# Kernel tuning notes

Measured on AMD Instinct MI355X. Metric: run time of the kernel, lower is better.

The kernel has to match this reference:

```python
import jax, jax.numpy as jnp
import numpy as np

N = 50000
E = 800000
HID = 128
EIN = 2 * HID + 1  # h[row] ++ h[col] ++ edge_attr
NC = 3             # n_coords
DIM = 3            # spatial dim
NORM_FACTOR = 100.0
LN_EPS = 1e-5


def layernorm(x, g, b):
    m = jnp.mean(x, axis=-1, keepdims=True)
    v = jnp.mean(jnp.square(x - m), axis=-1, keepdims=True)
    return (x - m) * jax.lax.rsqrt(v + LN_EPS) * g + b


def setup_inputs() -> dict:
    key = jax.random.key(0)
    ks = jax.random.split(key, 12)
    h = jax.random.normal(ks[0], (N, HID), dtype=jnp.float32)
    coord = jax.random.normal(ks[1], (N, NC, DIM), dtype=jnp.float32)
    coord_diff = jax.random.normal(ks[2], (E, NC, DIM), dtype=jnp.float32)
    edge_attr = jax.random.normal(ks[3], (E, 1), dtype=jnp.float32)
    edge_mask = jnp.ones((E, 1), dtype=jnp.float32)
    node_mask = jnp.ones((N, 1, 1), dtype=jnp.float32)
    row = jax.random.randint(ks[4], (E,), 0, N, dtype=jnp.int32)
    col = jax.random.randint(ks[5], (E,), 0, N, dtype=jnp.int32)
    # MLP params (stored [in, out])
    def xavier(k, fi, fo, gain=1.0):
        lim = gain * np.sqrt(6.0 / (fi + fo))
        return jax.random.uniform(k, (fi, fo), dtype=jnp.float32, minval=-lim, maxval=lim)
    W1 = xavier(ks[6], EIN, HID)
    b1 = jnp.zeros((HID,), jnp.float32)
    g1 = jnp.ones((HID,), jnp.float32)
    be1 = jnp.zeros((HID,), jnp.float32)
    W2 = xavier(ks[7], HID, HID)
    b2 = jnp.zeros((HID,), jnp.float32)
    g2 = jnp.ones((HID,), jnp.float32)
    be2 = jnp.zeros((HID,), jnp.float32)
    W3 = xavier(ks[8], HID, NC * NC, gain=0.01)  # final layer, no bias
    return dict(h=h, coord=coord, coord_diff=coord_diff, edge_attr=edge_attr,
                edge_mask=edge_mask, node_mask=node_mask, row=row, col=col,
                W1=W1, b1=b1, g1=g1, be1=be1, W2=W2, b2=b2, g2=g2, be2=be2, W3=W3)


def reference(h, coord, coord_diff, edge_attr, edge_mask, node_mask, row, col,
              W1, b1, g1, be1, W2, b2, g2, be2, W3):
    # gather node feats into edge features: [E, 2*HID + 1]
    x = jnp.concatenate([h[row], h[col], edge_attr], axis=1)
    x = jax.nn.silu(layernorm(x @ W1 + b1, g1, be1))
    x = jax.nn.silu(layernorm(x @ W2 + b2, g2, be2))
    phi = (x @ W3).reshape(-1, NC, NC)               # [E, NC, NC]
    trans = jnp.einsum('ejk,ejl->elk', coord_diff, phi)  # [E, NC, DIM]
    trans = trans * edge_mask[:, None]               # [E,1,1] broadcast
    agg = jax.ops.segment_sum(trans, row, num_segments=coord.shape[0]) / NORM_FACTOR
    return (coord + agg) * node_mask
```

## Files before the change

kernel.cpp:

```cpp
#include <hip/hip_runtime.h>
#include <hip/hip_bf16.h>

#define NN 50000
#define EE 800000

typedef __attribute__((ext_vector_type(8))) short short8;
typedef __attribute__((ext_vector_type(4))) float f32x4;

__device__ __forceinline__ float bf2f(ushort u) {
  union { unsigned u; float f; } v; v.u = ((unsigned)u) << 16; return v.f;
}
__device__ __forceinline__ ushort f2bf(float f) {
  union { float f; unsigned u; } v; v.f = f;
  unsigned r = v.u + 0x7FFFu + ((v.u >> 16) & 1u);
  return (ushort)(r >> 16);
}

__global__ void prep_kernel(const float* __restrict__ h, ushort* __restrict__ hb,
                            const float* __restrict__ W1, const float* __restrict__ W2,
                            const float* __restrict__ W3,
                            ushort* __restrict__ W1t, ushort* __restrict__ W2t,
                            ushort* __restrict__ W3t, float* __restrict__ agg) {
  int b = blockIdx.x, tid = threadIdx.x;
  if (b < 3125) {
    int i = b * 256 + tid;
    const float4* p = (const float4*)h;
    float4 a = p[2*i], c = p[2*i+1];
    short8 o;
    o[0]=f2bf(a.x); o[1]=f2bf(a.y); o[2]=f2bf(a.z); o[3]=f2bf(a.w);
    o[4]=f2bf(c.x); o[5]=f2bf(c.y); o[6]=f2bf(c.z); o[7]=f2bf(c.w);
    *(short8*)(hb + 8*i) = o;
  } else if (b < 3325) {
    int i = (b - 3125) * 256 + tid;
    if (i < 32768) {
      int n = i >> 8, k = i & 255;
      W1t[i] = f2bf(W1[k*128 + n]);
    } else if (i < 49152) {
      int j = i - 32768, n = j >> 7, k = j & 127;
      W2t[j] = f2bf(W2[k*128 + n]);
    } else if (i < 51200) {
      int j = i - 49152, n = j >> 7, k = j & 127;
      W3t[j] = (n < 9) ? f2bf(W3[k*9 + n]) : (ushort)0;
    }
  } else {
    int i = (b - 3325) * 256 + tid;
    if (i < NN*9) agg[i] = 0.f;
  }
}

__device__ __forceinline__ void ln_silu_inplace(ushort* smX, float* smRedS, float* smRedQ,
                                                const float* __restrict__ g,
                                                const float* __restrict__ be, int tid) {
  int e = tid & 63, w4 = tid >> 6, n0 = w4 * 32;
  float v[32]; float s = 0.f, q = 0.f;
  int bo[4];
  #pragma unroll
  for (int c = 0; c < 4; ++c) {
    bo[c] = (e*256 + (n0 + c*8)*2) ^ ((e & 7) << 4);
    short8 x = *(const short8*)((char*)smX + bo[c]);
    #pragma unroll
    for (int j = 0; j < 8; ++j) {
      float f = bf2f((ushort)x[j]); v[c*8+j] = f; s += f; q += f*f;
    }
  }
  smRedS[w4*64 + e] = s; smRedQ[w4*64 + e] = q;
  __syncthreads();
  s = smRedS[e] + smRedS[64+e] + smRedS[128+e] + smRedS[192+e];
  q = smRedQ[e] + smRedQ[64+e] + smRedQ[128+e] + smRedQ[192+e];
  float m  = s * (1.f/128.f);
  float rs = rsqrtf(q * (1.f/128.f) - m*m + 1e-5f);
  #pragma unroll
  for (int c = 0; c < 4; ++c) {
    short8 o;
    #pragma unroll
    for (int j = 0; j < 8; ++j) {
      float val = (v[c*8+j] - m) * rs * g[n0 + c*8 + j] + be[n0 + c*8 + j];
      val = val * __builtin_amdgcn_rcpf(1.f + __expf(-val));
      o[j] = f2bf(val);
    }
    *(short8*)((char*)smX + bo[c]) = o;
  }
  __syncthreads();
}

template<bool USE_HB>
__global__ __launch_bounds__(256, 4)
void edge_kernel(const float* __restrict__ h, const ushort* __restrict__ hb,
                 const ushort* __restrict__ W1t, const ushort* __restrict__ W2t,
                 const ushort* __restrict__ W3t,
                 const float* __restrict__ W1,
                 const float* __restrict__ b1, const float* __restrict__ g1, const float* __restrict__ be1,
                 const float* __restrict__ b2, const float* __restrict__ g2, const float* __restrict__ be2,
                 const float* __restrict__ edge_attr, const float* __restrict__ edge_mask,
                 const float* __restrict__ coord_diff,
                 const int* __restrict__ row, const int* __restrict__ col,
                 float* __restrict__ agg) {
  __shared__ __align__(16) char smem[35840];
  ushort* smA   = (ushort*)smem;
  ushort* smX   = (ushort*)smem;
  float*  smRedS = (float*)(smem + 16384);
  float*  smRedQ = (float*)(smem + 17408);
  float*  smPhi  = (float*)(smem + 18432);
  float*  smCd   = (float*)(smem + 32768);
  float*  smEA   = (float*)(smem + 35072);
  float*  smEM   = (float*)(smem + 35328);
  int*    smRow  = (int*)  (smem + 35584);

  const int tid  = threadIdx.x;
  const int lane = tid & 63;
  const int w    = tid >> 6;
  const int l15  = lane & 15;
  const int lh   = lane >> 4;
  const int wm   = w >> 1;
  const int wn   = w & 1;
  const int e0   = blockIdx.x * 64;

  {
    int e = tid >> 2, p = tid & 3;
    int re = row[e0 + e], ce = col[e0 + e];
    if (p == 0) { smEA[e] = edge_attr[e0+e]; smEM[e] = edge_mask[e0+e]; smRow[e] = re; }
    if (USE_HB) {
      const ushort* s = hb + (size_t)((p & 2) ? ce : re) * 128 + (p & 1) * 64;
      #pragma unroll
      for (int c = 0; c < 8; ++c) {
        short8 v = *(const short8*)(s + c*8);
        int bo = (e*512 + (p*8 + c)*16) ^ ((e & 7) << 4);
        *(short8*)((char*)smA + bo) = v;
      }
    } else {
      const float* s = h + (size_t)((p & 2) ? ce : re) * 128 + (p & 1) * 64;
      #pragma unroll
      for (int c = 0; c < 8; ++c) {
        float4 a = *(const float4*)(s + c*8);
        float4 bq = *(const float4*)(s + c*8 + 4);
        short8 v;
        v[0]=f2bf(a.x); v[1]=f2bf(a.y); v[2]=f2bf(a.z); v[3]=f2bf(a.w);
        v[4]=f2bf(bq.x); v[5]=f2bf(bq.y); v[6]=f2bf(bq.z); v[7]=f2bf(bq.w);
        int bo = (e*512 + (p*8 + c)*16) ^ ((e & 7) << 4);
        *(short8*)((char*)smA + bo) = v;
      }
    }
  }
  if (tid < 144)
    *(float4*)(smCd + tid*4) = *(const float4*)(coord_diff + (size_t)e0*9 + tid*4);
  __syncthreads();

  f32x4 acc[2][4] = {};
  {
    const ushort* Wp[4];
    #pragma unroll
    for (int nf = 0; nf < 4; ++nf)
      Wp[nf] = W1t + (size_t)(wn*64 + nf*16 + l15) * 256 + lh*8;
    #pragma unroll
    for (int k0 = 0; k0 < 8; ++k0) {
      short8 b[4];
      #pragma unroll
      for (int nf = 0; nf < 4; ++nf) b[nf] = *(const short8*)(Wp[nf] + k0*32);
      #pragma unroll
      for (int mi = 0; mi < 2; ++mi) {
        int r = wm*32 + mi*16 + l15;
        int bo = (r*512 + k0*64 + lh*16) ^ ((r & 7) << 4);
        short8 a = *(const short8*)((char*)smA + bo);
        #pragma unroll
        for (int nf = 0; nf < 4; ++nf)
          acc[mi][nf] = __builtin_amdgcn_mfma_f32_16x16x32_bf16(a, b[nf], acc[mi][nf], 0, 0, 0);
      }
    }
  }
  __syncthreads();

  {
    const float* w1last = W1 + 256*128;
    float bbv[4], wlv[4];
    #pragma unroll
    for (int nf = 0; nf < 4; ++nf) {
      int n = wn*64 + nf*16 + l15;
      bbv[nf] = b1[n]; wlv[nf] = w1last[n];
    }
    #pragma unroll
    for (int mi = 0; mi < 2; ++mi) {
      int r0 = wm*32 + mi*16 + lh*4;
      float ea[4];
      #pragma unroll
      for (int j = 0; j < 4; ++j) ea[j] = smEA[r0 + j];
      #pragma unroll
      for (int nf = 0; nf < 4; ++nf) {
        int n = wn*64 + nf*16 + l15;
        #pragma unroll
        for (int j = 0; j < 4; ++j) {
          int r = r0 + j;
          float val = acc[mi][nf][j] + bbv[nf] + ea[j] * wlv[nf];
          *(ushort*)((char*)smX + ((r*256 + n*2) ^ ((r & 7) << 4))) = f2bf(val);
        }
      }
    }
  }
  __syncthreads();
  ln_silu_inplace(smX, smRedS, smRedQ, g1, be1, tid);

  f32x4 acc2[2][4] = {};
  {
    const ushort* Wp[4];
    #pragma unroll
    for (int nf = 0; nf < 4; ++nf)
      Wp[nf] = W2t + (size_t)(wn*64 + nf*16 + l15) * 128 + lh*8;
    #pragma unroll
    for (int k0 = 0; k0 < 4; ++k0) {
      short8 b[4];
      #pragma unroll
      for (int nf = 0; nf < 4; ++nf) b[nf] = *(const short8*)(Wp[nf] + k0*32);
      #pragma unroll
      for (int mi = 0; mi < 2; ++mi) {
        int r = wm*32 + mi*16 + l15;
        int bo = (r*256 + k0*64 + lh*16) ^ ((r & 7) << 4);
        short8 a = *(const short8*)((char*)smX + bo);
        #pragma unroll
        for (int nf = 0; nf < 4; ++nf)
          acc2[mi][nf] = __builtin_amdgcn_mfma_f32_16x16x32_bf16(a, b[nf], acc2[mi][nf], 0, 0, 0);
      }
    }
  }
  __syncthreads();

  {
    float bbv[4];
    #pragma unroll
    for (int nf = 0; nf < 4; ++nf) bbv[nf] = b2[wn*64 + nf*16 + l15];
    #pragma unroll
    for (int mi = 0; mi < 2; ++mi) {
      int r0 = wm*32 + mi*16 + lh*4;
      #pragma unroll
      for (int nf = 0; nf < 4; ++nf) {
        int n = wn*64 + nf*16 + l15;
        #pragma unroll
        for (int j = 0; j < 4; ++j) {
          int r = r0 + j;
          float val = acc2[mi][nf][j] + bbv[nf];
          *(ushort*)((char*)smX + ((r*256 + n*2) ^ ((r & 7) << 4))) = f2bf(val);
        }
      }
    }
  }
  __syncthreads();
  ln_silu_inplace(smX, smRedS, smRedQ, g2, be2, tid);

  {
    f32x4 acc3 = {};
    const ushort* Wp = W3t + (size_t)l15*128 + lh*8;
    #pragma unroll
    for (int k0 = 0; k0 < 4; ++k0) {
      short8 b = *(const short8*)(Wp + k0*32);
      int r = w*16 + l15;
      int bo = (r*256 + k0*64 + lh*16) ^ ((r & 7) << 4);
      short8 a = *(const short8*)((char*)smX + bo);
      acc3 = __builtin_amdgcn_mfma_f32_16x16x32_bf16(a, b, acc3, 0, 0, 0);
    }
    if (l15 < 9) {
      #pragma unroll
      for (int j = 0; j < 4; ++j)
        smPhi[(w*16 + lh*4 + j)*12 + l15] = acc3[j];
    }
  }
  __syncthreads();

  {
    int e = tid >> 2, qd = tid & 3;
    int re = smRow[e];
    float em = smEM[e];
    const float* cd = smCd + e*9;
    const float* ph = smPhi + e*12;
    for (int idx = qd; idx < 9; idx += 4) {
      int l2 = idx / 3, k = idx - l2*3;
      float t = cd[k]*ph[l2] + cd[3+k]*ph[3+l2] + cd[6+k]*ph[6+l2];
      unsafeAtomicAdd(&agg[(size_t)re*9 + idx], t * em);
    }
  }
}

__global__ void finalize_kernel(const float* __restrict__ coord, const float* __restrict__ node_mask,
                                const float* __restrict__ agg, float* __restrict__ out) {
  int i = blockIdx.x * 256 + threadIdx.x;
  if (i < NN*9) {
    int n = i / 9;
    out[i] = (coord[i] + agg[i] * 0.01f) * node_mask[n];
  }
}

extern "C" void kernel_launch(void* const* d_in, const int* in_sizes, int n_in,
                              void* d_out, int out_size, void* d_ws, size_t ws_size,
                              hipStream_t stream) {
  const float* h          = (const float*)d_in[0];
  const float* coord      = (const float*)d_in[1];
  const float* coord_diff = (const float*)d_in[2];
  const float* edge_attr  = (const float*)d_in[3];
  const float* edge_mask  = (const float*)d_in[4];
  const float* node_mask  = (const float*)d_in[5];
  const int*   rowi       = (const int*)d_in[6];
  const int*   coli       = (const int*)d_in[7];
  const float* W1  = (const float*)d_in[8];
  const float* b1  = (const float*)d_in[9];
  const float* g1  = (const float*)d_in[10];
  const float* be1 = (const float*)d_in[11];
  const float* W2  = (const float*)d_in[12];
  const float* b2  = (const float*)d_in[13];
  const float* g2  = (const float*)d_in[14];
  const float* be2 = (const float*)d_in[15];
  const float* W3  = (const float*)d_in[16];

  char* ws = (char*)d_ws;
  float*  agg = (float*)ws;
  ushort* W1t = (ushort*)(ws + 1800064);
  ushort* W2t = (ushort*)(ws + 1865600);
  ushort* W3t = (ushort*)(ws + 1898368);
  ushort* hb  = (ushort*)(ws + 1902464);
  bool use_hb = ws_size >= (size_t)1902464 + 12800000;

  if (use_hb) {
    prep_kernel<<<3325 + (NN*9 + 255)/256, 256, 0, stream>>>(h, hb, W1, W2, W3, W1t, W2t, W3t, agg);
    edge_kernel<true><<<EE/64, 256, 0, stream>>>(h, hb, W1t, W2t, W3t, W1,
        b1, g1, be1, b2, g2, be2, edge_attr, edge_mask, coord_diff, rowi, coli, agg);
  } else {
    prep_kernel<<<3325 + (NN*9 + 255)/256, 256, 0, stream>>>(h, hb, W1, W2, W3, W1t, W2t, W3t, agg);
    edge_kernel<false><<<EE/64, 256, 0, stream>>>(h, hb, W1t, W2t, W3t, W1,
        b1, g1, be1, b2, g2, be2, edge_attr, edge_mask, coord_diff, rowi, coli, agg);
  }
  finalize_kernel<<<(NN*9 + 255)/256, 256, 0, stream>>>(coord, node_mask, agg, (float*)d_out);
}
```

Baseline: 519.7 us.

## Transpose MFMA roles and fuse bias/LayerNorm/SiLU into register epilogues

The MLP GEMMs are re-oriented so weights become the A operand (read from global) and edge activations the B operand from LDS. Each lane then holds four consecutive hidden features per edge. That lets the bias, edge-attr term, LayerNorm statistics and SiLU run directly on accumulator registers, with shuffle reductions and a small cross-wave LDS exchange. This removes the separate bf16 round-trip through LDS before each LayerNorm and several block barriers. The cost is more global weight loads per wave and a different LDS access pattern for the activations.

```diff
diff --git a/kernel.cpp b/kernel.cpp
--- a/kernel.cpp
+++ b/kernel.cpp
@@ -5,6 +5,7 @@
 #define EE 800000
 
 typedef __attribute__((ext_vector_type(8))) short short8;
+typedef __attribute__((ext_vector_type(4))) short short4v;
 typedef __attribute__((ext_vector_type(4))) float f32x4;
 
 __device__ __forceinline__ float bf2f(ushort u) {
@@ -14,6 +15,9 @@
   union { float f; unsigned u; } v; v.f = f;
   unsigned r = v.u + 0x7FFFu + ((v.u >> 16) & 1u);
   return (ushort)(r >> 16);
+}
+__device__ __forceinline__ float silu(float v) {
+  return v * __builtin_amdgcn_rcpf(1.f + __expf(-v));
 }
 
 __global__ void prep_kernel(const float* __restrict__ h, ushort* __restrict__ hb,
@@ -48,41 +52,6 @@
   }
 }
 
-__device__ __forceinline__ void ln_silu_inplace(ushort* smX, float* smRedS, float* smRedQ,
-                                                const float* __restrict__ g,
-                                                const float* __restrict__ be, int tid) {
-  int e = tid & 63, w4 = tid >> 6, n0 = w4 * 32;
-  float v[32]; float s = 0.f, q = 0.f;
-  int bo[4];
-  #pragma unroll
-  for (int c = 0; c < 4; ++c) {
-    bo[c] = (e*256 + (n0 + c*8)*2) ^ ((e & 7) << 4);
-    short8 x = *(const short8*)((char*)smX + bo[c]);
-    #pragma unroll
-    for (int j = 0; j < 8; ++j) {
-      float f = bf2f((ushort)x[j]); v[c*8+j] = f; s += f; q += f*f;
-    }
-  }
-  smRedS[w4*64 + e] = s; smRedQ[w4*64 + e] = q;
-  __syncthreads();
-  s = smRedS[e] + smRedS[64+e] + smRedS[128+e] + smRedS[192+e];
-  q = smRedQ[e] + smRedQ[64+e] + smRedQ[128+e] + smRedQ[192+e];
-  float m  = s * (1.f/128.f);
-  float rs = rsqrtf(q * (1.f/128.f) - m*m + 1e-5f);
-  #pragma unroll
-  for (int c = 0; c < 4; ++c) {
-    short8 o;
-    #pragma unroll
-    for (int j = 0; j < 8; ++j) {
-      float val = (v[c*8+j] - m) * rs * g[n0 + c*8 + j] + be[n0 + c*8 + j];
-      val = val * __builtin_amdgcn_rcpf(1.f + __expf(-val));
-      o[j] = f2bf(val);
-    }
-    *(short8*)((char*)smX + bo[c]) = o;
-  }
-  __syncthreads();
-}
-
 template<bool USE_HB>
 __global__ __launch_bounds__(256, 4)
 void edge_kernel(const float* __restrict__ h, const ushort* __restrict__ hb,
@@ -95,16 +64,15 @@
                  const float* __restrict__ coord_diff,
                  const int* __restrict__ row, const int* __restrict__ col,
                  float* __restrict__ agg) {
-  __shared__ __align__(16) char smem[35840];
+  __shared__ __align__(16) char smem[36864];
   ushort* smA   = (ushort*)smem;
   ushort* smX   = (ushort*)smem;
-  float*  smRedS = (float*)(smem + 16384);
-  float*  smRedQ = (float*)(smem + 17408);
-  float*  smPhi  = (float*)(smem + 18432);
-  float*  smCd   = (float*)(smem + 32768);
-  float*  smEA   = (float*)(smem + 35072);
-  float*  smEM   = (float*)(smem + 35328);
-  int*    smRow  = (int*)  (smem + 35584);
+  float*  smPhi = (float*)(smem + 16384);
+  float*  smCd  = (float*)(smem + 32768);
+  float*  smEA  = (float*)(smem + 35072);
+  float*  smEM  = (float*)(smem + 35328);
+  int*    smRow = (int*)  (smem + 35584);
+  float2* smRed = (float2*)(smem + 35840);
 
   const int tid  = threadIdx.x;
   const int lane = tid & 63;
@@ -115,6 +83,8 @@
   const int wn   = w & 1;
   const int e0   = blockIdx.x * 64;
 
+  const int nb = wm*64 + lh*4;
+
   {
     int e = tid >> 2, p = tid & 3;
     int re = row[e0 + e], ce = col[e0 + e];
@@ -145,121 +115,175 @@
     *(float4*)(smCd + tid*4) = *(const float4*)(coord_diff + (size_t)e0*9 + tid*4);
   __syncthreads();
 
-  f32x4 acc[2][4] = {};
-  {
-    const ushort* Wp[4];
-    #pragma unroll
-    for (int nf = 0; nf < 4; ++nf)
-      Wp[nf] = W1t + (size_t)(wn*64 + nf*16 + l15) * 256 + lh*8;
+  f32x4 acc[4][2] = {};
+  {
+    const ushort* A0 = W1t + (size_t)(wm*64 + l15) * 256 + lh*8;
     #pragma unroll
     for (int k0 = 0; k0 < 8; ++k0) {
-      short8 b[4];
-      #pragma unroll
-      for (int nf = 0; nf < 4; ++nf) b[nf] = *(const short8*)(Wp[nf] + k0*32);
-      #pragma unroll
-      for (int mi = 0; mi < 2; ++mi) {
-        int r = wm*32 + mi*16 + l15;
-        int bo = (r*512 + k0*64 + lh*16) ^ ((r & 7) << 4);
-        short8 a = *(const short8*)((char*)smA + bo);
-        #pragma unroll
-        for (int nf = 0; nf < 4; ++nf)
-          acc[mi][nf] = __builtin_amdgcn_mfma_f32_16x16x32_bf16(a, b[nf], acc[mi][nf], 0, 0, 0);
-      }
-    }
-  }
-  __syncthreads();
-
-  {
-    const float* w1last = W1 + 256*128;
-    float bbv[4], wlv[4];
-    #pragma unroll
-    for (int nf = 0; nf < 4; ++nf) {
-      int n = wn*64 + nf*16 + l15;
-      bbv[nf] = b1[n]; wlv[nf] = w1last[n];
-    }
-    #pragma unroll
-    for (int mi = 0; mi < 2; ++mi) {
-      int r0 = wm*32 + mi*16 + lh*4;
-      float ea[4];
-      #pragma unroll
-      for (int j = 0; j < 4; ++j) ea[j] = smEA[r0 + j];
-      #pragma unroll
-      for (int nf = 0; nf < 4; ++nf) {
-        int n = wn*64 + nf*16 + l15;
+      short8 a[4], b[2];
+      #pragma unroll
+      for (int mf = 0; mf < 4; ++mf) a[mf] = *(const short8*)(A0 + mf*4096 + k0*32);
+      #pragma unroll
+      for (int nf = 0; nf < 2; ++nf) {
+        int e = wn*32 + nf*16 + l15;
+        int bo = (e*512 + k0*64 + lh*16) ^ ((e & 7) << 4);
+        b[nf] = *(const short8*)((char*)smA + bo);
+      }
+      #pragma unroll
+      for (int mf = 0; mf < 4; ++mf)
+        #pragma unroll
+        for (int nf = 0; nf < 2; ++nf)
+          acc[mf][nf] = __builtin_amdgcn_mfma_f32_16x16x32_bf16(a[mf], b[nf], acc[mf][nf], 0, 0, 0);
+    }
+  }
+
+  float s[2] = {0.f, 0.f}, q[2] = {0.f, 0.f};
+  {
+    const float* wl = W1 + 256*128;
+    float ea[2];
+    #pragma unroll
+    for (int nf = 0; nf < 2; ++nf) ea[nf] = smEA[wn*32 + nf*16 + l15];
+    #pragma unroll
+    for (int mf = 0; mf < 4; ++mf) {
+      float4 b1q = *(const float4*)(b1 + nb + mf*16);
+      float4 wlq = *(const float4*)(wl + nb + mf*16);
+      #pragma unroll
+      for (int nf = 0; nf < 2; ++nf)
         #pragma unroll
         for (int j = 0; j < 4; ++j) {
-          int r = r0 + j;
-          float val = acc[mi][nf][j] + bbv[nf] + ea[j] * wlv[nf];
-          *(ushort*)((char*)smX + ((r*256 + n*2) ^ ((r & 7) << 4))) = f2bf(val);
+          float t = acc[mf][nf][j] + ((const float*)&b1q)[j] + ea[nf] * ((const float*)&wlq)[j];
+          acc[mf][nf][j] = t; s[nf] += t; q[nf] += t*t;
         }
-      }
-    }
-  }
-  __syncthreads();
-  ln_silu_inplace(smX, smRedS, smRedQ, g1, be1, tid);
-
-  f32x4 acc2[2][4] = {};
-  {
-    const ushort* Wp[4];
-    #pragma unroll
-    for (int nf = 0; nf < 4; ++nf)
-      Wp[nf] = W2t + (size_t)(wn*64 + nf*16 + l15) * 128 + lh*8;
+    }
+  }
+  #pragma unroll
+  for (int nf = 0; nf < 2; ++nf) {
+    s[nf] += __shfl_xor(s[nf], 16, 64); s[nf] += __shfl_xor(s[nf], 32, 64);
+    q[nf] += __shfl_xor(q[nf], 16, 64); q[nf] += __shfl_xor(q[nf], 32, 64);
+  }
+  if (lh == 0) {
+    #pragma unroll
+    for (int nf = 0; nf < 2; ++nf)
+      smRed[((wm*2 + wn)*2 + nf)*16 + l15] = make_float2(s[nf], q[nf]);
+  }
+  __syncthreads();
+
+  {
+    float m[2], rs[2];
+    #pragma unroll
+    for (int nf = 0; nf < 2; ++nf) {
+      float2 po = smRed[(((wm^1)*2 + wn)*2 + nf)*16 + l15];
+      float S = s[nf] + po.x, Q = q[nf] + po.y;
+      m[nf] = S * (1.f/128.f);
+      rs[nf] = rsqrtf(Q * (1.f/128.f) - m[nf]*m[nf] + 1e-5f);
+    }
+    #pragma unroll
+    for (int mf = 0; mf < 4; ++mf) {
+      float4 gq  = *(const float4*)(g1 + nb + mf*16);
+      float4 beq = *(const float4*)(be1 + nb + mf*16);
+      #pragma unroll
+      for (int nf = 0; nf < 2; ++nf) {
+        int e = wn*32 + nf*16 + l15;
+        short4v o;
+        #pragma unroll
+        for (int j = 0; j < 4; ++j) {
+          float val = (acc[mf][nf][j] - m[nf]) * rs[nf] * ((const float*)&gq)[j] + ((const float*)&beq)[j];
+          o[j] = f2bf(silu(val));
+        }
+        int bo = (e*256 + (nb + mf*16)*2) ^ ((e & 7) << 4);
+        *(short4v*)((char*)smX + bo) = o;
+      }
+    }
+  }
+  __syncthreads();
+
+  f32x4 acc2[4][2] = {};
+  {
+    const ushort* A2 = W2t + (size_t)(wm*64 + l15) * 128 + lh*8;
     #pragma unroll
     for (int k0 = 0; k0 < 4; ++k0) {
-      short8 b[4];
-      #pragma unroll
-      for (int nf = 0; nf < 4; ++nf) b[nf] = *(const short8*)(Wp[nf] + k0*32);
-      #pragma unroll
-      for (int mi = 0; mi < 2; ++mi) {
-        int r = wm*32 + mi*16 + l15;
-        int bo = (r*256 + k0*64 + lh*16) ^ ((r & 7) << 4);
-        short8 a = *(const short8*)((char*)smX + bo);
-        #pragma unroll
-        for (int nf = 0; nf < 4; ++nf)
-          acc2[mi][nf] = __builtin_amdgcn_mfma_f32_16x16x32_bf16(a, b[nf], acc2[mi][nf], 0, 0, 0);
-      }
-    }
-  }
-  __syncthreads();
-
-  {
-    float bbv[4];
-    #pragma unroll
-    for (int nf = 0; nf < 4; ++nf) bbv[nf] = b2[wn*64 + nf*16 + l15];
-    #pragma unroll
-    for (int mi = 0; mi < 2; ++mi) {
-      int r0 = wm*32 + mi*16 + lh*4;
-      #pragma unroll
-      for (int nf = 0; nf < 4; ++nf) {
-        int n = wn*64 + nf*16 + l15;
+      short8 a[4], b[2];
+      #pragma unroll
+      for (int mf = 0; mf < 4; ++mf) a[mf] = *(const short8*)(A2 + mf*2048 + k0*32);
+      #pragma unroll
+      for (int nf = 0; nf < 2; ++nf) {
+        int e = wn*32 + nf*16 + l15;
+        int bo = (e*256 + k0*64 + lh*16) ^ ((e & 7) << 4);
+        b[nf] = *(const short8*)((char*)smX + bo);
+      }
+      #pragma unroll
+      for (int mf = 0; mf < 4; ++mf)
+        #pragma unroll
+        for (int nf = 0; nf < 2; ++nf)
+          acc2[mf][nf] = __builtin_amdgcn_mfma_f32_16x16x32_bf16(a[mf], b[nf], acc2[mf][nf], 0, 0, 0);
+    }
+  }
+
+  float s2[2] = {0.f, 0.f}, q2[2] = {0.f, 0.f};
+  #pragma unroll
+  for (int mf = 0; mf < 4; ++mf) {
+    float4 b2q = *(const float4*)(b2 + nb + mf*16);
+    #pragma unroll
+    for (int nf = 0; nf < 2; ++nf)
+      #pragma unroll
+      for (int j = 0; j < 4; ++j) {
+        float t = acc2[mf][nf][j] + ((const float*)&b2q)[j];
+        acc2[mf][nf][j] = t; s2[nf] += t; q2[nf] += t*t;
+      }
+  }
+  #pragma unroll
+  for (int nf = 0; nf < 2; ++nf) {
+    s2[nf] += __shfl_xor(s2[nf], 16, 64); s2[nf] += __shfl_xor(s2[nf], 32, 64);
+    q2[nf] += __shfl_xor(q2[nf], 16, 64); q2[nf] += __shfl_xor(q2[nf], 32, 64);
+  }
+  if (lh == 0) {
+    #pragma unroll
+    for (int nf = 0; nf < 2; ++nf)
+      smRed[((wm*2 + wn)*2 + nf)*16 + l15] = make_float2(s2[nf], q2[nf]);
+  }
+  __syncthreads();
+
+  {
+    float m[2], rs[2];
+    #pragma unroll
+    for (int nf = 0; nf < 2; ++nf) {
+      float2 po = smRed[(((wm^1)*2 + wn)*2 + nf)*16 + l15];
+      float S = s2[nf] + po.x, Q = q2[nf] + po.y;
+      m[nf] = S * (1.f/128.f);
+      rs[nf] = rsqrtf(Q * (1.f/128.f) - m[nf]*m[nf] + 1e-5f);
+    }
+    #pragma unroll
+    for (int mf = 0; mf < 4; ++mf) {
+      float4 gq  = *(const float4*)(g2 + nb + mf*16);
+      float4 beq = *(const float4*)(be2 + nb + mf*16);
+      #pragma unroll
+      for (int nf = 0; nf < 2; ++nf) {
+        int e = wn*32 + nf*16 + l15;
+        short4v o;
         #pragma unroll
         for (int j = 0; j < 4; ++j) {
-          int r = r0 + j;
-          float val = acc2[mi][nf][j] + bbv[nf];
-          *(ushort*)((char*)smX + ((r*256 + n*2) ^ ((r & 7) << 4))) = f2bf(val);
+          float val = (acc2[mf][nf][j] - m[nf]) * rs[nf] * ((const float*)&gq)[j] + ((const float*)&beq)[j];
+          o[j] = f2bf(silu(val));
         }
-      }
-    }
-  }
-  __syncthreads();
-  ln_silu_inplace(smX, smRedS, smRedQ, g2, be2, tid);
+        int bo = (e*256 + (nb + mf*16)*2) ^ ((e & 7) << 4);
+        *(short4v*)((char*)smX + bo) = o;
+      }
+    }
+  }
+  __syncthreads();
 
   {
     f32x4 acc3 = {};
-    const ushort* Wp = W3t + (size_t)l15*128 + lh*8;
+    const ushort* A3 = W3t + (size_t)l15 * 128 + lh*8;
+    int e = w*16 + l15;
     #pragma unroll
     for (int k0 = 0; k0 < 4; ++k0) {
-      short8 b = *(const short8*)(Wp + k0*32);
-      int r = w*16 + l15;
-      int bo = (r*256 + k0*64 + lh*16) ^ ((r & 7) << 4);
-      short8 a = *(const short8*)((char*)smX + bo);
+      short8 a = *(const short8*)(A3 + k0*32);
+      int bo = (e*256 + k0*64 + lh*16) ^ ((e & 7) << 4);
+      short8 b = *(const short8*)((char*)smX + bo);
       acc3 = __builtin_amdgcn_mfma_f32_16x16x32_bf16(a, b, acc3, 0, 0, 0);
     }
-    if (l15 < 9) {
-      #pragma unroll
-      for (int j = 0; j < 4; ++j)
-        smPhi[(w*16 + lh*4 + j)*12 + l15] = acc3[j];
-    }
+    *(float4*)(smPhi + e*20 + lh*4) = *(float4*)&acc3;
   }
   __syncthreads();
 
@@ -268,7 +292,7 @@
     int re = smRow[e];
     float em = smEM[e];
     const float* cd = smCd + e*9;
-    const float* ph = smPhi + e*12;
+    const float* ph = smPhi + e*20;
     for (int idx = qd; idx < 9; idx += 4) {
       int l2 = idx / 3, k = idx - l2*3;
       float t = cd[k]*ph[l2] + cd[3+k]*ph[3+l2] + cd[6+k]*ph[6+l2];
@@ -315,12 +339,11 @@
   ushort* hb  = (ushort*)(ws + 1902464);
   bool use_hb = ws_size >= (size_t)1902464 + 12800000;
 
+  prep_kernel<<<3325 + (NN*9 + 255)/256, 256, 0, stream>>>(h, hb, W1, W2, W3, W1t, W2t, W3t, agg);
   if (use_hb) {
-    prep_kernel<<<3325 + (NN*9 + 255)/256, 256, 0, stream>>>(h, hb, W1, W2, W3, W1t, W2t, W3t, agg);
     edge_kernel<true><<<EE/64, 256, 0, stream>>>(h, hb, W1t, W2t, W3t, W1,
         b1, g1, be1, b2, g2, be2, edge_attr, edge_mask, coord_diff, rowi, coli, agg);
   } else {
-    prep_kernel<<<3325 + (NN*9 + 255)/256, 256, 0, stream>>>(h, hb, W1, W2, W3, W1t, W2t, W3t, agg);
     edge_kernel<false><<<EE/64, 256, 0, stream>>>(h, hb, W1t, W2t, W3t, W1,
         b1, g1, be1, b2, g2, be2, edge_attr, edge_mask, coord_diff, rowi, coli, agg);
   }
```

After: 508.8 us. 2.1% less time.
